# Kernel tuning notes

Measured on AMD Instinct MI355X. Metric: run time of the kernel, lower is better.

The kernel has to match this reference:

```python
import jax, jax.numpy as jnp
import numpy as np

PS = 8          # patch size
D_STATE = 16
D_CONV = 4
DT_RANK = 6     # ceil(96/16)
N_HEADS = 2
NEG = jnp.float32(-1e30)
_DIRS = np.array([[-1, 0], [1, 0], [0, -1], [0, 1]], np.int32)


def _ln(x, w, b, eps=1e-5):
    mu = x.mean(-1, keepdims=True)
    var = ((x - mu) ** 2).mean(-1, keepdims=True)
    return (x - mu) * jax.lax.rsqrt(var + eps) * w + b


def _vit_score_map(x, pos_embed, proj_w, proj_b, in_w, in_b, out_w, out_b,
                   ln1_w, ln1_b, ff1_w, ff1_b, ff2_w, ff2_b, ln2_w, ln2_b,
                   score_w, score_b):
    B, C, H, W = x.shape
    Hp, Wp = H // PS, W // PS
    N = Hp * Wp
    E = proj_w.shape[0]
    # F.unfold ordering: per patch the vector is (C, kr, kc) flattened
    patches = x.reshape(B, C, Hp, PS, Wp, PS).transpose(0, 2, 4, 1, 3, 5).reshape(B, N, C * PS * PS)
    patches = patches @ proj_w.T + proj_b
    if pos_embed.shape[1] != N:
        o = int(pos_embed.shape[1] ** 0.5)
        pe = jax.image.resize(pos_embed.reshape(1, o, o, E), (1, Hp, Wp, E), 'bilinear').reshape(1, N, E)
    else:
        pe = pos_embed
    patches = patches + 0.1 * pe
    # nn.TransformerEncoderLayer defaults: post-norm, ReLU, eval (no dropout)
    qkv = patches @ in_w.T + in_b
    q, k, v = jnp.split(qkv, 3, axis=-1)
    dh = E // N_HEADS
    def heads(t):
        return t.reshape(B, N, N_HEADS, dh).transpose(0, 2, 1, 3)
    q, k, v = heads(q), heads(k), heads(v)
    attn = jax.nn.softmax(jnp.einsum('bhqd,bhkd->bhqk', q, k) / np.float32(np.sqrt(dh)), axis=-1)
    ctx = jnp.einsum('bhqk,bhkd->bhqd', attn, v).transpose(0, 2, 1, 3).reshape(B, N, E)
    src = _ln(patches + (ctx @ out_w.T + out_b), ln1_w, ln1_b)
    ff = jax.nn.relu(src @ ff1_w.T + ff1_b) @ ff2_w.T + ff2_b
    src = _ln(src + ff, ln2_w, ln2_b)
    scores = jax.nn.sigmoid((src @ score_w.T + score_b)[..., 0])
    pvar = patches.var(axis=-1, ddof=1)          # torch.var is unbiased
    final = 0.7 * scores + 0.3 * jax.nn.sigmoid(pvar * 10.0)
    return final.reshape(B, Hp, Wp)


def _traversal(score):
    """Greedy adaptive patch traversal: start at global argmax, walk to the best
    unvisited 4-neighbor; on dead-end jump to the global argmax over unvisited."""
    Hp, Wp = score.shape
    n = Hp * Wp
    s = score.reshape(-1)
    dirs = jnp.asarray(_DIRS)
    start = jnp.argmax(s).astype(jnp.int32)
    visited0 = jnp.zeros((n,), bool).at[start].set(True)

    def step(carry, _):
        visited, cur = carry
        ci, cj = cur // Wp, cur % Wp
        ni, nj = ci + dirs[:, 0], cj + dirs[:, 1]
        valid = (ni >= 0) & (ni < Hp) & (nj >= 0) & (nj < Wp)
        nidx = (jnp.clip(ni, 0, Hp - 1) * Wp + jnp.clip(nj, 0, Wp - 1)).astype(jnp.int32)
        nsc = jnp.where(valid & ~visited[nidx], s[nidx], NEG)
        b = jnp.argmax(nsc)                       # first-max tie-break == '>' loop order
        jump = jnp.argmax(jnp.where(visited, NEG, s)).astype(jnp.int32)
        nxt = jnp.where(nsc[b] > NEG * 0.5, nidx[b], jump).astype(jnp.int32)
        return (visited.at[nxt].set(True), nxt), nxt

    _, rest = jax.lax.scan(step, (visited0, start), None, length=n - 1)
    return jnp.concatenate([start[None], rest])


def _mamba(u, in_w, conv_w, conv_b, xproj_w, dt_w, dt_b, A_log, D_skip, out_w):
    B, L, _ = u.shape
    d_in = conv_w.shape[0]
    xz = u @ in_w.T                               # (B,L,2*d_in)
    xx, z = jnp.split(xz, 2, axis=-1)
    # causal depthwise conv over sequence
    xc = jnp.pad(xx.transpose(0, 2, 1), ((0, 0), (0, 0), (D_CONV - 1, 0)))
    xc = jax.lax.conv_general_dilated(xc, conv_w, (1,), 'VALID',
                                      feature_group_count=d_in,
                                      dimension_numbers=('NCH', 'OIH', 'NCH'))
    xx = jax.nn.silu((xc + conv_b[None, :, None]).transpose(0, 2, 1))   # (B,L,d_in)
    dbl = xx @ xproj_w.T
    dt, Bm, Cm = jnp.split(dbl, [DT_RANK, DT_RANK + D_STATE], axis=-1)
    dt = jax.nn.softplus(dt @ dt_w.T + dt_b)      # (B,L,d_in)
    A = -jnp.exp(A_log)                           # (d_in, d_state)

    def step(h, inp):
        dt_t, B_t, C_t, x_t = inp                 # (B,d_in),(B,ds),(B,ds),(B,d_in)
        h = jnp.exp(dt_t[..., None] * A) * h + (dt_t * x_t)[..., None] * B_t[:, None, :]
        return h, jnp.einsum('bds,bs->bd', h, C_t)

    h0 = jnp.zeros((B, d_in, D_STATE), u.dtype)
    xs = (dt.transpose(1, 0, 2), Bm.transpose(1, 0, 2), Cm.transpose(1, 0, 2), xx.transpose(1, 0, 2))
    _, ys = jax.lax.scan(step, h0, xs)
    y = ys.transpose(1, 0, 2) + xx * D_skip
    return (y * jax.nn.silu(z)) @ out_w.T


def setup_inputs() -> dict:
    key = jax.random.key(0)
    ks = jax.random.split(key, 20)
    B, C, H, W = 2, 96, 128, 128
    E, FF = 96, 2048
    d_in, dr, ds, dc = 192, 6, 16, 4
    f32 = jnp.float32
    def w(k, shape, s=0.02):
        return jax.random.normal(k, shape, f32) * s
    return dict(
        x=jax.random.normal(ks[0], (B, C, H, W), f32),
        pe=w(ks[1], (B, H * W, C), 0.02),
        pos_embed=w(ks[2], (1, 784, E)),
        vit_proj_w=w(ks[3], (E, C * PS * PS)),
        vit_proj_b=jnp.zeros((E,), f32),
        attn_in_w=w(ks[4], (3 * E, E)),
        attn_in_b=jnp.zeros((3 * E,), f32),
        attn_out_w=w(ks[5], (E, E)),
        attn_out_b=jnp.zeros((E,), f32),
        ln1_w=jnp.ones((E,), f32), ln1_b=jnp.zeros((E,), f32),
        ff1_w=w(ks[6], (FF, E)), ff1_b=jnp.zeros((FF,), f32),
        ff2_w=w(ks[7], (E, FF)), ff2_b=jnp.zeros((E,), f32),
        ln2_w=jnp.ones((E,), f32), ln2_b=jnp.zeros((E,), f32),
        score_w=w(ks[8], (1, E)), score_b=jnp.zeros((1,), f32),
        norm_w=jnp.ones((C,), f32), norm_b=jnp.zeros((C,), f32),
        in_proj_w=w(ks[9], (2 * d_in, C)),
        conv_w=w(ks[10], (d_in, 1, dc), 0.1),
        conv_b=jnp.zeros((d_in,), f32),
        x_proj_w=w(ks[11], (dr + 2 * ds, d_in)),
        dt_w=w(ks[12], (d_in, dr)),
        dt_b=jnp.full((d_in,), -4.6, f32),        # softplus(dt_b) ~ 0.01 (mamba dt init)
        A_log=jnp.log(jnp.tile(jnp.arange(1, ds + 1, dtype=f32), (d_in, 1))),
        D_skip=jnp.ones((d_in,), f32),
        out_proj_w=w(ks[13], (C, d_in)),
    )


def reference(x, pe, pos_embed, vit_proj_w, vit_proj_b, attn_in_w, attn_in_b,
              attn_out_w, attn_out_b, ln1_w, ln1_b, ff1_w, ff1_b, ff2_w, ff2_b,
              ln2_w, ln2_b, score_w, score_b, norm_w, norm_b, in_proj_w,
              conv_w, conv_b, x_proj_w, dt_w, dt_b, A_log, D_skip, out_proj_w):
    B, C, H, W = x.shape
    n = H * W
    # Dynamic_Adaptive_Scan with the code's DCNv3Function-is-None fallback:
    # x = input_last, permuted back to channels-first => identity on x.
    x_adapted = x
    score_map = _vit_score_map(x_adapted, pos_embed, vit_proj_w, vit_proj_b,
                               attn_in_w, attn_in_b, attn_out_w, attn_out_b,
                               ln1_w, ln1_b, ff1_w, ff1_b, ff2_w, ff2_b,
                               ln2_w, ln2_b, score_w, score_b)
    order = jax.vmap(_traversal)(jax.lax.stop_gradient(score_map))    # (B, Hp*Wp)
    Hp, Wp = score_map.shape[1], score_map.shape[2]
    pi, pj = order // Wp, order % Wp
    # expand each patch into its PSxPS pixels in raster order
    offs = (jnp.arange(PS, dtype=jnp.int32)[:, None] * W + jnp.arange(PS, dtype=jnp.int32)[None, :]).reshape(-1)
    idx = ((pi * PS * W + pj * PS)[..., None] + offs).reshape(B, n)    # (B, n)
    x_tok = jnp.take_along_axis(x_adapted.reshape(B, C, n), idx[:, None, :], axis=2).transpose(0, 2, 1)
    pe_r = jnp.take_along_axis(pe, idx[..., None], axis=1)
    tokens = _ln(x_tok + pe_r, norm_w, norm_b)
    y = _mamba(tokens, in_proj_w, conv_w, conv_b, x_proj_w, dt_w, dt_b, A_log, D_skip, out_proj_w)
    # scatter back to spatial raster order
    out = jax.vmap(lambda yb, ib: jnp.zeros_like(yb).at[ib].set(yb))(y, idx)
    return out.transpose(0, 2, 1).reshape(B, C, H, W)
```

## Files before the change

### kernel.cpp

```cpp
#include <hip/hip_runtime.h>
#include <math.h>

#define BB 2
#define CC 96
#define HH 128
#define WW 128
#define PS 8
#define HP 16
#define WP 16
#define NPATCH 256
#define EE 96
#define FF 2048
#define DH 48
#define DIN 192
#define DR 6
#define DS 16
#define LL 16384
#define NCHUNK 512
#define CLEN 32
#define NSEG 16
#define SEGC 32
#define KTOT 6144
#define KSPLIT 32
#define KSL 192

__device__ __forceinline__ float sigmoid_acc(float x){ return 1.f/(1.f+expf(-x)); }
__device__ __forceinline__ float sigmoid_fast(float x){ return 1.f/(1.f+__expf(-x)); }

__global__ void k_resize_pe(const float* __restrict__ pos, float* __restrict__ pe16){
  int n = blockIdx.x;
  int oi = n / WP, oj = n % WP;
  int e = threadIdx.x;
  const float inv = 1.75f;
  float sfi = (oi + 0.5f)*inv - 0.5f;
  float sfj = (oj + 0.5f)*inv - 0.5f;
  int i0 = max(0, (int)ceilf(sfi - inv)), i1 = min(27, (int)floorf(sfi + inv));
  int j0 = max(0, (int)ceilf(sfj - inv)), j1 = min(27, (int)floorf(sfj + inv));
  float si = 0.f, sj = 0.f;
  for(int j=i0;j<=i1;j++) si += fmaxf(0.f, 1.f - fabsf(sfi - (float)j)/inv);
  for(int j=j0;j<=j1;j++) sj += fmaxf(0.f, 1.f - fabsf(sfj - (float)j)/inv);
  float acc = 0.f;
  for(int ji=i0;ji<=i1;ji++){
    float wv = fmaxf(0.f, 1.f - fabsf(sfi - (float)ji)/inv) / si;
    for(int jj=j0;jj<=j1;jj++){
      float wu = fmaxf(0.f, 1.f - fabsf(sfj - (float)jj)/inv);
      acc += wv * (wu/sj) * pos[(ji*28+jj)*EE + e];
    }
  }
  pe16[n*EE + e] = acc;
}

__global__ void k_wtr(const float* __restrict__ vw, float* __restrict__ Wt){
  __shared__ float t[64*97];
  int k0 = blockIdx.x*64;
  int tid = threadIdx.x;
  for(int i=tid;i<64*EE;i+=256){
    int e = i>>6, kk = i&63;
    t[kk*97 + e] = vw[(size_t)e*KTOT + k0 + kk];
  }
  __syncthreads();
  for(int i=tid;i<64*EE;i+=256){
    int kk = i/EE, e = i%EE;
    Wt[(size_t)(k0+kk)*EE + e] = t[kk*97 + e];
  }
}

__global__ __launch_bounds__(384) void k_pproj(const float* __restrict__ x,
    const float* __restrict__ Wt, float* __restrict__ part){
  __shared__ float As[16*196];
  int bidx = blockIdx.x;
  int ks = bidx & (KSPLIT-1);
  int pb = bidx >> 5;
  int b = pb >> 4, pi = pb & 15;
  int c0 = ks*3;
  int tid = threadIdx.x;
  for(int i=tid;i<24*128;i+=384){
    int row = i>>7;
    int col = i&127;
    int cl = row>>3, dr = row&7;
    float v = x[(((size_t)(b*CC + c0+cl))<<14) + (size_t)((pi*PS+dr)<<7) + col];
    As[(col>>3)*196 + cl*64 + dr*8 + (col&7)] = v;
  }
  __syncthreads();
  int e = tid % EE;
  int pq = tid / EE;
  const float* wp = Wt + (size_t)(ks*KSL)*EE + e;
  float acc0=0.f, acc1=0.f, acc2=0.f, acc3=0.f;
  const float4* A0 = (const float4*)(As + (pq*4+0)*196);
  const float4* A1 = (const float4*)(As + (pq*4+1)*196);
  const float4* A2 = (const float4*)(As + (pq*4+2)*196);
  const float4* A3 = (const float4*)(As + (pq*4+3)*196);
  #pragma unroll 4
  for(int k4=0;k4<48;k4++){
    float w0 = wp[(k4*4+0)*EE];
    float w1 = wp[(k4*4+1)*EE];
    float w2 = wp[(k4*4+2)*EE];
    float w3 = wp[(k4*4+3)*EE];
    float4 a;
    a = A0[k4]; acc0 += a.x*w0 + a.y*w1 + a.z*w2 + a.w*w3;
    a = A1[k4]; acc1 += a.x*w0 + a.y*w1 + a.z*w2 + a.w*w3;
    a = A2[k4]; acc2 += a.x*w0 + a.y*w1 + a.z*w2 + a.w*w3;
    a = A3[k4]; acc3 += a.x*w0 + a.y*w1 + a.z*w2 + a.w*w3;
  }
  size_t gp0 = (size_t)b*NPATCH + pi*WP + pq*4;
  part[((size_t)ks*512 + gp0+0)*EE + e] = acc0;
  part[((size_t)ks*512 + gp0+1)*EE + e] = acc1;
  part[((size_t)ks*512 + gp0+2)*EE + e] = acc2;
  part[((size_t)ks*512 + gp0+3)*EE + e] = acc3;
}

__global__ __launch_bounds__(320) void k_preduce_qkv(const float* __restrict__ part,
    const float* __restrict__ pb, const float* __restrict__ pe16,
    const float* __restrict__ inw, const float* __restrict__ inb,
    float* __restrict__ patches, float* __restrict__ pvar, float* __restrict__ qkv){
  int gp = blockIdx.x;
  int n = gp % NPATCH;
  int tid = threadIdx.x;
  __shared__ float a[EE];
  __shared__ float ps[2], pq2[2];
  float v = 0.f;
  if(tid < EE){
    float s = 0.f;
    #pragma unroll 8
    for(int ks=0;ks<KSPLIT;ks++) s += part[((size_t)ks*512 + gp)*EE + tid];
    v = s + pb[tid] + 0.1f*pe16[n*EE + tid];
    a[tid] = v;
    patches[(size_t)gp*EE + tid] = v;
  }
  if(tid < 128){
    float sv = v, sq = v*v;
    for(int off=32; off>0; off>>=1){ sv += __shfl_xor(sv, off); sq += __shfl_xor(sq, off); }
    if((tid&63)==0){ ps[tid>>6]=sv; pq2[tid>>6]=sq; }
  }
  __syncthreads();
  if(tid==0){
    float s = ps[0]+ps[1], qq = pq2[0]+pq2[1];
    float mu = s/EE;
    pvar[gp] = (qq - EE*mu*mu)/(EE-1);
  }
  if(tid < 288){
    const float4* ar = (const float4*)a;
    const float4* wr = (const float4*)(inw + (size_t)tid*EE);
    float4 s4 = {0.f,0.f,0.f,0.f};
    #pragma unroll
    for(int k=0;k<24;k++){
      float4 av=ar[k], wv=wr[k];
      s4.x += av.x*wv.x; s4.y += av.y*wv.y; s4.z += av.z*wv.z; s4.w += av.w*wv.w;
    }
    qkv[(size_t)gp*288 + tid] = inb[tid] + (s4.x+s4.y)+(s4.z+s4.w);
  }
}

__global__ __launch_bounds__(256) void k_attn_ln1(const float* __restrict__ qkv,
    const float* __restrict__ ow, const float* __restrict__ ob,
    const float* __restrict__ patches, const float* __restrict__ lw,
    const float* __restrict__ lb, float* __restrict__ src1){
  int gb = blockIdx.x;
  int i = gb & 255, b = gb >> 8;
  int tid = threadIdx.x;
  __shared__ float q[EE];
  __shared__ float2 red[NPATCH];
  __shared__ float p0[NPATCH], p1[NPATCH];
  __shared__ float part[2][EE];
  __shared__ float ctxs[EE];
  __shared__ float ps[2], pq2[2], st[2];
  const float* base = qkv + (size_t)b*NPATCH*288;
  if(tid < EE) q[tid] = base[(size_t)i*288 + tid];
  __syncthreads();
  float sc0, sc1;
  {
    const float4* krow = (const float4*)(base + (size_t)tid*288 + 96);
    const float4* q4 = (const float4*)q;
    float4 a0 = {0.f,0.f,0.f,0.f}, a1 = {0.f,0.f,0.f,0.f};
    #pragma unroll
    for(int k=0;k<12;k++){
      float4 kv=krow[k], qv=q4[k];
      a0.x += qv.x*kv.x; a0.y += qv.y*kv.y; a0.z += qv.z*kv.z; a0.w += qv.w*kv.w;
    }
    #pragma unroll
    for(int k=12;k<24;k++){
      float4 kv=krow[k], qv=q4[k];
      a1.x += qv.x*kv.x; a1.y += qv.y*kv.y; a1.z += qv.z*kv.z; a1.w += qv.w*kv.w;
    }
    sc0 = ((a0.x+a0.y)+(a0.z+a0.w)) * 0.14433756729740643f;
    sc1 = ((a1.x+a1.y)+(a1.z+a1.w)) * 0.14433756729740643f;
  }
  red[tid] = make_float2(sc0, sc1); __syncthreads();
  for(int stp=128; stp>0; stp>>=1){
    if(tid<stp){ float2 o=red[tid+stp]; red[tid].x=fmaxf(red[tid].x,o.x); red[tid].y=fmaxf(red[tid].y,o.y); }
    __syncthreads();
  }
  float2 mx = red[0]; __syncthreads();
  float ev0 = expf(sc0 - mx.x), ev1 = expf(sc1 - mx.y);
  red[tid] = make_float2(ev0, ev1); __syncthreads();
  for(int stp=128; stp>0; stp>>=1){
    if(tid<stp){ float2 o=red[tid+stp]; red[tid].x+=o.x; red[tid].y+=o.y; }
    __syncthreads();
  }
  float2 dn = red[0]; __syncthreads();
  p0[tid] = ev0/dn.x; p1[tid] = ev1/dn.y;
  __syncthreads();
  if(tid < 192){
    int dd = tid % EE, jh = tid / EE;
    const float* vb = base + 192 + dd;
    const float* pp = (dd < DH) ? p0 : p1;
    float acc0 = 0.f, acc1 = 0.f;
    #pragma unroll 4
    for(int j=jh*128; j<jh*128+128; j+=2){
      acc0 += pp[j]*vb[(size_t)j*288];
      acc1 += pp[j+1]*vb[(size_t)(j+1)*288];
    }
    part[jh][dd] = acc0+acc1;
  }
  __syncthreads();
  if(tid < EE) ctxs[tid] = part[0][tid] + part[1][tid];
  __syncthreads();
  float o = 0.f;
  if(tid < EE){
    const float4* ar = (const float4*)ctxs;
    const float4* wr = (const float4*)(ow + (size_t)tid*EE);
    float4 s4 = {0.f,0.f,0.f,0.f};
    #pragma unroll
    for(int k=0;k<24;k++){
      float4 av=ar[k], wv=wr[k];
      s4.x += av.x*wv.x; s4.y += av.y*wv.y; s4.z += av.z*wv.z; s4.w += av.w*wv.w;
    }
    o = ob[tid] + (s4.x+s4.y)+(s4.z+s4.w) + patches[(size_t)gb*EE + tid];
  }
  if(tid < 128){
    float sv = o, sq = o*o;
    for(int off=32; off>0; off>>=1){ sv += __shfl_xor(sv, off); sq += __shfl_xor(sq, off); }
    if((tid&63)==0){ ps[tid>>6]=sv; pq2[tid>>6]=sq; }
  }
  __syncthreads();
  if(tid==0){
    float s = ps[0]+ps[1], qq = pq2[0]+pq2[1];
    float mu = s/EE;
    st[0]=mu; st[1]=rsqrtf(qq/EE - mu*mu + 1e-5f);
  }
  __syncthreads();
  if(tid < EE) src1[(size_t)gb*EE + tid] = (o-st[0])*st[1]*lw[tid] + lb[tid];
}

__global__ __launch_bounds__(512) void k_ff1(const float* __restrict__ src1,
    const float* __restrict__ w1, const float* __restrict__ b1, float* __restrict__ ffh){
  int row0 = blockIdx.x*2; int tid = threadIdx.x;
  const float4* a0 = (const float4*)(src1 + (size_t)row0*EE);
  const float4* a1 = (const float4*)(src1 + (size_t)(row0+1)*EE);
  for(int fo=0;fo<4;fo++){
    int f = fo*512 + tid;
    const float4* wr = (const float4*)(w1 + (size_t)f*EE);
    float bc = b1[f];
    float acc0=bc, acc1=bc;
    #pragma unroll
    for(int k=0;k<24;k++){
      float4 wv = wr[k];
      float4 av;
      av = a0[k]; acc0 += av.x*wv.x+av.y*wv.y+av.z*wv.z+av.w*wv.w;
      av = a1[k]; acc1 += av.x*wv.x+av.y*wv.y+av.z*wv.z+av.w*wv.w;
    }
    ffh[(size_t)(row0+0)*FF + f] = fmaxf(acc0, 0.f);
    ffh[(size_t)(row0+1)*FF + f] = fmaxf(acc1, 0.f);
  }
}

__global__ __launch_bounds__(384) void k_ff2_score(const float* __restrict__ ffh,
    const float* __restrict__ w2, const float* __restrict__ b2,
    const float* __restrict__ src1, const float* __restrict__ lw,
    const float* __restrict__ lb, const float* __restrict__ sw,
    const float* __restrict__ sb, const float* __restrict__ pvar,
    float* __restrict__ fscore){
  __shared__ float partl[8][EE];
  __shared__ float s2[2][EE];
  __shared__ float psr[2][2], pqr[2][2], str[2][2];
  int row0 = blockIdx.x*2; int tid = threadIdx.x;
  int e = tid % EE, fg = tid / EE;
  const float4* wr = (const float4*)(w2 + (size_t)e*FF + fg*512);
  const float4* h0 = (const float4*)(ffh + (size_t)row0*FF + fg*512);
  const float4* h1 = (const float4*)(ffh + (size_t)(row0+1)*FF + fg*512);
  float acc0=0.f, acc1=0.f;
  #pragma unroll 4
  for(int k=0;k<128;k++){
    float4 wv = wr[k];
    float4 hv;
    hv = h0[k]; acc0 += hv.x*wv.x+hv.y*wv.y+hv.z*wv.z+hv.w*wv.w;
    hv = h1[k]; acc1 += hv.x*wv.x+hv.y*wv.y+hv.z*wv.z+hv.w*wv.w;
  }
  partl[0*4+fg][e] = acc0;
  partl[1*4+fg][e] = acc1;
  __syncthreads();
  if(tid < 192){
    int r = tid / EE, e2 = tid % EE;
    float s = partl[r*4+0][e2] + partl[r*4+1][e2] + partl[r*4+2][e2] + partl[r*4+3][e2];
    s2[r][e2] = s + b2[e2] + src1[(size_t)(row0+r)*EE + e2];
  }
  __syncthreads();
  int g = tid >> 7, t = tid & 127;
  float v = 0.f;
  if(g < 2){
    v = (t < EE) ? s2[g][t] : 0.f;
    float sv = v, sq = v*v;
    for(int off=32; off>0; off>>=1){ sv += __shfl_xor(sv, off); sq += __shfl_xor(sq, off); }
    if((t&63)==0){ psr[g][t>>6]=sv; pqr[g][t>>6]=sq; }
  }
  __syncthreads();
  if(g < 2 && t == 0){
    float s = psr[g][0]+psr[g][1], qq = pqr[g][0]+pqr[g][1];
    float mu = s/EE;
    str[g][0]=mu; str[g][1]=rsqrtf(qq/EE - mu*mu + 1e-5f);
  }
  __syncthreads();
  if(g < 2){
    float o = (t < EE) ? ((v-str[g][0])*str[g][1]*lw[t] + lb[t]) * sw[t] : 0.f;
    for(int off=32; off>0; off>>=1) o += __shfl_xor(o, off);
    if((t&63)==0) psr[g][t>>6] = o;
  }
  __syncthreads();
  if(g < 2 && t == 0){
    float acc = psr[g][0]+psr[g][1] + sb[0];
    fscore[row0+g] = 0.7f*sigmoid_acc(acc) + 0.3f*sigmoid_acc(pvar[row0+g]*10.f);
  }
}

__global__ void k_traversal(const float* __restrict__ fscore, int* __restrict__ order){
  int b = blockIdx.x; int lane = threadIdx.x;
  __shared__ float fsl[NPATCH];
  __shared__ int   sidxl[NPATCH];
  __shared__ int   ordl[NPATCH];
  for(int k=lane;k<NPATCH;k+=64) fsl[k] = fscore[b*NPATCH+k];
  __syncthreads();
  {
    float s0=fsl[lane], s1=fsl[64+lane], s2=fsl[128+lane], s3=fsl[192+lane];
    int i0=lane, i1=64+lane, i2=128+lane, i3=192+lane;
    int c0=0,c1=0,c2=0,c3=0;
    for(int j=0;j<NPATCH;j++){
      float sj=fsl[j];
      c0 += (sj>s0 || (sj==s0 && j<i0)) ? 1:0;
      c1 += (sj>s1 || (sj==s1 && j<i1)) ? 1:0;
      c2 += (sj>s2 || (sj==s2 && j<i2)) ? 1:0;
      c3 += (sj>s3 || (sj==s3 && j<i3)) ? 1:0;
    }
    sidxl[c0]=i0; sidxl[c1]=i1; sidxl[c2]=i2; sidxl[c3]=i3;
  }
  __syncthreads();
  if(lane==0){
    int cur = sidxl[0];
    ordl[0] = cur;
    fsl[cur] = -1e30f;
    int ptr = 1;
    int jcand = sidxl[1];
    for(int step=1; step<NPATCH; step++){
      int ci = cur>>4, cj = cur&15;
      int a0 = (ci>0)  ? cur-16 : cur;
      int a1 = (ci<15) ? cur+16 : cur;
      int a2 = (cj>0)  ? cur-1  : cur;
      int a3 = (cj<15) ? cur+1  : cur;
      float n0 = fsl[a0];
      float n1 = fsl[a1];
      float n2 = fsl[a2];
      float n3 = fsl[a3];
      float bv = n0; int bi = a0;
      if(n1 > bv){ bv=n1; bi=a1; }
      if(n2 > bv){ bv=n2; bi=a2; }
      if(n3 > bv){ bv=n3; bi=a3; }
      int nxt = (bv > -1e29f) ? bi : jcand;
      fsl[nxt] = -1e30f;
      ordl[step] = nxt;
      cur = nxt;
      if(nxt == jcand && step < NPATCH-1){
        float jv;
        do { ptr++; jcand = sidxl[ptr]; jv = fsl[jcand]; } while(jv <= -1e29f);
      }
    }
  }
  __syncthreads();
  for(int k=lane;k<NPATCH;k+=64) order[b*NPATCH+k] = ordl[k];
}

__global__ __launch_bounds__(256) void k_gather_ln(const float* __restrict__ x,
    const float* __restrict__ pe, const int* __restrict__ order,
    const float* __restrict__ nw, const float* __restrict__ nb,
    float* __restrict__ tokens){
  __shared__ float val[64*97];
  int gb = blockIdx.x; int b = gb >> 8; int r = gb & 255;
  int tid = threadIdx.x;
  int p = order[b*NPATCH + r]; int pi = p>>4, pj = p&15;
  for(int i=tid;i<96*64;i+=256){
    int c = i>>6, q = i&63;
    int dr = q>>3, dc = q&7;
    val[q*97 + c] = x[(((size_t)(b*CC + c))<<14) + (size_t)((pi*PS+dr)<<7) + pj*PS + dc];
  }
  __syncthreads();
  for(int i=tid;i<64*EE;i+=256){
    int q = i/EE, c = i%EE;
    int pix = ((pi*PS + (q>>3))<<7) + pj*PS + (q&7);
    val[q*97 + c] += pe[((size_t)b*(HH*WW) + pix)*CC + c];
  }
  __syncthreads();
  int wid = tid>>6, lane = tid&63;
  for(int t=wid; t<64; t+=4){
    float v1 = val[t*97 + lane];
    float v2 = (lane<32) ? val[t*97 + 64 + lane] : 0.f;
    float sv = v1+v2, sq = v1*v1 + v2*v2;
    for(int off=32; off>0; off>>=1){ sv += __shfl_xor(sv, off); sq += __shfl_xor(sq, off); }
    float mu = sv/EE;
    float rs = rsqrtf(sq/EE - mu*mu + 1e-5f);
    size_t tb = ((size_t)b*LL + r*64 + t)*EE;
    tokens[tb + lane] = (v1-mu)*rs*nw[lane] + nb[lane];
    if(lane < 32) tokens[tb + 64 + lane] = (v2-mu)*rs*nw[64+lane] + nb[64+lane];
  }
}

__global__ __launch_bounds__(768, 5) void k_inproj_conv(const float* __restrict__ tokens,
    const float* __restrict__ w, const float* __restrict__ cw, const float* __restrict__ cb,
    float* __restrict__ z, float* __restrict__ xc){
  __shared__ float a[35*EE];
  __shared__ float ps[12*384];
  __shared__ float xxl[35*DIN];
  int rb = blockIdx.x; size_t row0 = (size_t)rb*32;
  int l0 = (int)(row0 % LL);
  int tid = threadIdx.x;
  int kh = tid / 384;
  int col = tid - kh*384;
  {
    const float4* src = (const float4*)(tokens + (row0-3)*EE);
    float4* adst = (float4*)a;
    for(int idx=tid; idx<840; idx+=768){
      float4 v;
      if(l0==0 && idx<72){ v.x=0.f; v.y=0.f; v.z=0.f; v.w=0.f; }
      else v = src[idx];
      adst[idx] = v;
    }
  }
  float4 wv[12];
  const float4* wr4 = (const float4*)(w + (size_t)col*EE + kh*48);
  #pragma unroll
  for(int i=0;i<12;i++) wv[i] = wr4[i];
  __syncthreads();
  #pragma unroll
  for(int g=0; g<3; g++){
    float acc[12];
    #pragma unroll
    for(int r=0;r<12;r++){
      int gi = g*12 + r;
      if(gi < 35){
        const float4* ar = (const float4*)(a + gi*EE + kh*48);
        float4 s4 = {0.f,0.f,0.f,0.f};
        #pragma unroll
        for(int i=0;i<12;i++){
          float4 av = ar[i];
          s4.x += av.x*wv[i].x; s4.y += av.y*wv[i].y; s4.z += av.z*wv[i].z; s4.w += av.w*wv[i].w;
        }
        acc[r] = (s4.x+s4.y)+(s4.z+s4.w);
      } else acc[r] = 0.f;
    }
    if(kh==1){
      #pragma unroll
      for(int r=0;r<12;r++) if(g*12+r < 35) ps[r*384 + col] = acc[r];
    }
    __syncthreads();
    if(kh==0){
      #pragma unroll
      for(int r=0;r<12;r++){
        int gi = g*12 + r;
        if(gi < 35){
          float tot = acc[r] + ps[r*384 + col];
          if(col < DIN) xxl[gi*DIN + col] = tot;
          else if(gi >= 3) z[(row0 + gi - 3)*DIN + (col - DIN)] = tot;
        }
      }
    }
    __syncthreads();
  }
  #pragma unroll
  for(int it=0; it<8; it++){
    int idx = tid + it*768;
    int rr = idx / DIN, d = idx - rr*DIN;
    float v = cb[d]
      + cw[d*4+0]*xxl[(rr+0)*DIN + d]
      + cw[d*4+1]*xxl[(rr+1)*DIN + d]
      + cw[d*4+2]*xxl[(rr+2)*DIN + d]
      + cw[d*4+3]*xxl[(rr+3)*DIN + d];
    xc[(row0 + rr)*DIN + d] = v * sigmoid_fast(v);
  }
}

__global__ __launch_bounds__(320) void k_xproj(const float* __restrict__ xc, const float* __restrict__ xpw,
    const float* __restrict__ dtw, const float* __restrict__ dtb,
    float* __restrict__ dt, float* __restrict__ Bm, float* __restrict__ Cm){
  __shared__ float a[8][196];
  __shared__ float dbl[8][40];
  int rb = blockIdx.x; size_t row0 = (size_t)rb*8;
  int tid = threadIdx.x;
  for(int i=tid;i<8*DIN;i+=320){ int r=i/DIN, k=i%DIN; a[r][k] = xc[(row0+r)*DIN + k]; }
  __syncthreads();
  {
    int r = tid & 7, o = tid >> 3;
    if(o < 38){
      const float4* wr = (const float4*)(xpw + (size_t)o*DIN);
      const float4* ar = (const float4*)(a[r]);
      float4 s4 = {0.f,0.f,0.f,0.f};
      #pragma unroll
      for(int k=0;k<48;k++){
        float4 av=ar[k], wv=wr[k];
        s4.x += av.x*wv.x; s4.y += av.y*wv.y; s4.z += av.z*wv.z; s4.w += av.w*wv.w;
      }
      dbl[r][o] = (s4.x+s4.y)+(s4.z+s4.w);
    }
  }
  __syncthreads();
  for(int t=tid;t<8*DIN;t+=320){
    int r = t/DIN, d = t%DIN;
    float acc = dtb[d];
    #pragma unroll
    for(int j=0;j<DR;j++) acc += dbl[r][j]*dtw[d*DR+j];
    dt[(row0+r)*DIN + d] = fmaxf(acc, 0.f) + log1pf(__expf(-fabsf(acc)));
  }
  if(tid < 8*DS){
    int r = tid/DS, s = tid%DS;
    Bm[(row0+r)*DS + s] = dbl[r][6+s];
    Cm[(row0+r)*DS + s] = dbl[r][22+s];
  }
}

__global__ __launch_bounds__(192) void k_scan1(const float* __restrict__ dt,
    const float* __restrict__ xc, const float* __restrict__ Bm,
    const float* __restrict__ Alog, float* __restrict__ hend, float* __restrict__ sumdt){
  int blk = blockIdx.x;
  int b = blk >> 9, c = blk & (NCHUNK-1);
  int d = threadIdx.x;
  float A[16];
  {
    const float4* a4 = (const float4*)(Alog + d*DS);
    #pragma unroll
    for(int i=0;i<4;i++){
      float4 v = a4[i];
      A[i*4+0]=-expf(v.x); A[i*4+1]=-expf(v.y); A[i*4+2]=-expf(v.z); A[i*4+3]=-expf(v.w);
    }
  }
  float h[16];
  #pragma unroll
  for(int s=0;s<16;s++) h[s]=0.f;
  float sd = 0.f;
  size_t base = (size_t)b*LL + (size_t)c*CLEN;
  const float* dp = dt + base*DIN + d;
  const float* xp = xc + base*DIN + d;
  const float4* bp = (const float4*)(Bm + base*DS);
  for(int t=0;t<CLEN;t++){
    float dtv = dp[(size_t)t*DIN];
    float xv  = xp[(size_t)t*DIN];
    float4 b0=bp[t*4+0], b1=bp[t*4+1], b2=bp[t*4+2], b3=bp[t*4+3];
    float e[16];
    #pragma unroll
    for(int s=0;s<16;s++) e[s] = __expf(dtv*A[s]);
    float Bv[16] = {b0.x,b0.y,b0.z,b0.w,b1.x,b1.y,b1.z,b1.w,b2.x,b2.y,b2.z,b2.w,b3.x,b3.y,b3.z,b3.w};
    float dx = dtv*xv; sd += dtv;
    #pragma unroll
    for(int s=0;s<16;s++) h[s] = e[s]*h[s] + dx*Bv[s];
  }
  size_t o = ((size_t)c*BB + b)*DIN + d;
  float4* hp = (float4*)(hend + o*DS);
  hp[0] = make_float4(h[0],h[1],h[2],h[3]);
  hp[1] = make_float4(h[4],h[5],h[6],h[7]);
  hp[2] = make_float4(h[8],h[9],h[10],h[11]);
  hp[3] = make_float4(h[12],h[13],h[14],h[15]);
  sumdt[o] = sd;
}

__global__ __launch_bounds__(256) void k_scan2a(const float* __restrict__ hend,
    const float* __restrict__ sumdt, const float* __restrict__ Alog,
    float* __restrict__ segP, float* __restrict__ segH){
  int g = blockIdx.x*256 + threadIdx.x;
  int seg = g / 6144; int r = g % 6144;
  int b = r / 3072; int d = (r % 3072) >> 4; int s = r & 15;
  float A = -expf(Alog[d*DS + s]);
  float P = 1.f, H = 0.f;
  int c0 = seg*SEGC;
  for(int cc=0; cc<SEGC; cc+=4){
    float sd[4], he[4];
    #pragma unroll
    for(int j=0;j<4;j++){
      size_t o = ((size_t)(c0+cc+j)*BB + b)*DIN + d;
      sd[j] = sumdt[o]; he[j] = hend[o*DS + s];
    }
    #pragma unroll
    for(int j=0;j<4;j++){
      float aa = __expf(A*sd[j]);
      H = aa*H + he[j]; P *= aa;
    }
  }
  segP[seg*6144 + r] = P; segH[seg*6144 + r] = H;
}

__global__ void k_scan2b(const float* __restrict__ segP, const float* __restrict__ segH,
                         float* __restrict__ segHin){
  int r = blockIdx.x*256 + threadIdx.x;
  float P[NSEG], H[NSEG];
  #pragma unroll
  for(int sg=0; sg<NSEG; sg++){ P[sg]=segP[sg*6144+r]; H[sg]=segH[sg*6144+r]; }
  float h = 0.f;
  #pragma unroll
  for(int sg=0; sg<NSEG; sg++){
    segHin[sg*6144 + r] = h;
    h = P[sg]*h + H[sg];
  }
}

__global__ __launch_bounds__(256) void k_scan2c(float* __restrict__ hend,
    const float* __restrict__ sumdt, const float* __restrict__ Alog,
    const float* __restrict__ segHin){
  int g = blockIdx.x*256 + threadIdx.x;
  int seg = g / 6144; int r = g % 6144;
  int b = r / 3072; int d = (r % 3072) >> 4; int s = r & 15;
  float A = -expf(Alog[d*DS + s]);
  float h = segHin[seg*6144 + r];
  int c0 = seg*SEGC;
  for(int cc=0; cc<SEGC; cc+=4){
    float sd[4], he[4]; size_t oo[4];
    #pragma unroll
    for(int j=0;j<4;j++){
      oo[j] = ((size_t)(c0+cc+j)*BB + b)*DIN + d;
      sd[j] = sumdt[oo[j]]; he[j] = hend[oo[j]*DS + s];
    }
    #pragma unroll
    for(int j=0;j<4;j++){
      hend[oo[j]*DS + s] = h;
      float aa = __expf(A*sd[j]);
      h = aa*h + he[j];
    }
  }
}

__global__ __launch_bounds__(192) void k_scan3(const float* __restrict__ dt,
    const float* __restrict__ xc, const float* __restrict__ Bm, const float* __restrict__ Cm,
    const float* __restrict__ Alog, const float* __restrict__ hin,
    const float* __restrict__ Dskip, float* __restrict__ zg){
  int blk = blockIdx.x;
  int b = blk >> 9, c = blk & (NCHUNK-1);
  int d = threadIdx.x;
  float A[16];
  {
    const float4* a4 = (const float4*)(Alog + d*DS);
    #pragma unroll
    for(int i=0;i<4;i++){
      float4 v = a4[i];
      A[i*4+0]=-expf(v.x); A[i*4+1]=-expf(v.y); A[i*4+2]=-expf(v.z); A[i*4+3]=-expf(v.w);
    }
  }
  size_t o = ((size_t)c*BB + b)*DIN + d;
  float h[16];
  {
    const float4* hi = (const float4*)(hin + o*DS);
    #pragma unroll
    for(int i=0;i<4;i++){
      float4 v = hi[i];
      h[i*4+0]=v.x; h[i*4+1]=v.y; h[i*4+2]=v.z; h[i*4+3]=v.w;
    }
  }
  float Dv = Dskip[d];
  size_t base = (size_t)b*LL + (size_t)c*CLEN;
  const float* dp = dt + base*DIN + d;
  const float* xp = xc + base*DIN + d;
  float* zp = zg + base*DIN + d;
  const float4* bp = (const float4*)(Bm + base*DS);
  const float4* cp = (const float4*)(Cm + base*DS);
  for(int t=0;t<CLEN;t++){
    float dtv = dp[(size_t)t*DIN];
    float xv  = xp[(size_t)t*DIN];
    float zv  = zp[(size_t)t*DIN];
    float4 b0=bp[t*4+0], b1=bp[t*4+1], b2=bp[t*4+2], b3=bp[t*4+3];
    float4 c0=cp[t*4+0], c1=cp[t*4+1], c2=cp[t*4+2], c3=cp[t*4+3];
    float e[16];
    #pragma unroll
    for(int s=0;s<16;s++) e[s] = __expf(dtv*A[s]);
    float Bv[16] = {b0.x,b0.y,b0.z,b0.w,b1.x,b1.y,b1.z,b1.w,b2.x,b2.y,b2.z,b2.w,b3.x,b3.y,b3.z,b3.w};
    float Cv[16] = {c0.x,c0.y,c0.z,c0.w,c1.x,c1.y,c1.z,c1.w,c2.x,c2.y,c2.z,c2.w,c3.x,c3.y,c3.z,c3.w};
    float dx = dtv*xv;
    float y = 0.f;
    #pragma unroll
    for(int s=0;s<16;s++){ h[s] = e[s]*h[s] + dx*Bv[s]; y += h[s]*Cv[s]; }
    float yy = y + xv*Dv;
    zp[(size_t)t*DIN] = yy * (zv * sigmoid_fast(zv));
  }
}

__global__ __launch_bounds__(384) void k_outproj(const float* __restrict__ g,
    const float* __restrict__ w, float* __restrict__ ytok){
  __shared__ float a[16*DIN];
  __shared__ float psA[16*EE];
  __shared__ float psB[16*EE];
  int rb = blockIdx.x; size_t row0 = (size_t)rb*16;
  int tid = threadIdx.x;
  int col = tid % EE, kq = tid / EE;
  {
    const float4* src = (const float4*)(g + row0*DIN);
    float4* ad = (float4*)a;
    ad[tid] = src[tid];
    ad[tid+384] = src[tid+384];
  }
  float4 wv[12];
  const float4* wr4 = (const float4*)(w + (size_t)col*DIN + kq*48);
  #pragma unroll
  for(int i=0;i<12;i++) wv[i] = wr4[i];
  __syncthreads();
  float acc[16];
  for(int r=0;r<16;r++){
    const float4* ar = (const float4*)(a + r*DIN + kq*48);
    float4 s4 = {0.f,0.f,0.f,0.f};
    #pragma unroll
    for(int i=0;i<12;i++){
      float4 av = ar[i];
      s4.x += av.x*wv[i].x; s4.y += av.y*wv[i].y; s4.z += av.z*wv[i].z; s4.w += av.w*wv[i].w;
    }
    acc[r] = (s4.x+s4.y)+(s4.z+s4.w);
  }
  if(kq==1){
    for(int r=0;r<16;r++) psA[r*EE+col] = acc[r];
  }
  if(kq==3){
    for(int r=0;r<16;r++) psB[r*EE+col] = acc[r];
  }
  __syncthreads();
  if(kq==0){
    for(int r=0;r<16;r++) acc[r] += psA[r*EE+col];
  }
  if(kq==2){
    for(int r=0;r<16;r++) acc[r] += psB[r*EE+col];
  }
  __syncthreads();
  if(kq==2){
    for(int r=0;r<16;r++) psA[r*EE+col] = acc[r];
  }
  __syncthreads();
  if(kq==0){
    for(int r=0;r<16;r++) ytok[(row0+r)*EE + col] = acc[r] + psA[r*EE+col];
  }
}

__global__ __launch_bounds__(256) void k_scatter(const float* __restrict__ ytok,
    const int* __restrict__ order, float* __restrict__ out){
  __shared__ float yt[64*100];
  int gb = blockIdx.x; int b = gb>>8, r = gb&255;
  int p = order[b*NPATCH + r]; int pi = p>>4, pj = p&15;
  int tid = threadIdx.x;
  for(int i=tid;i<64*24;i+=256){
    int q = i/24, c4 = i%24;
    float4 v = ((const float4*)(ytok + ((size_t)b*LL + r*64 + q)*EE))[c4];
    ((float4*)(yt + q*100))[c4] = v;
  }
  __syncthreads();
  int q = tid&63; int cg = tid>>6;
  int pix = ((pi*PS + (q>>3))<<7) + pj*PS + (q&7);
  for(int c=cg;c<CC;c+=4){
    out[(((size_t)(b*CC + c))<<14) + pix] = yt[q*100 + c];
  }
}

extern "C" void kernel_launch(void* const* d_in, const int* in_sizes, int n_in,
                              void* d_out, int out_size, void* d_ws, size_t ws_size,
                              hipStream_t stream){
  (void)in_sizes; (void)n_in; (void)out_size; (void)ws_size;
  const float* x    = (const float*)d_in[0];
  const float* pe   = (const float*)d_in[1];
  const float* pos  = (const float*)d_in[2];
  const float* vw   = (const float*)d_in[3];
  const float* vb   = (const float*)d_in[4];
  const float* inw  = (const float*)d_in[5];
  const float* inb  = (const float*)d_in[6];
  const float* ow   = (const float*)d_in[7];
  const float* ob   = (const float*)d_in[8];
  const float* l1w  = (const float*)d_in[9];
  const float* l1b  = (const float*)d_in[10];
  const float* f1w  = (const float*)d_in[11];
  const float* f1b  = (const float*)d_in[12];
  const float* f2w  = (const float*)d_in[13];
  const float* f2b  = (const float*)d_in[14];
  const float* l2w  = (const float*)d_in[15];
  const float* l2b  = (const float*)d_in[16];
  const float* sw   = (const float*)d_in[17];
  const float* sb   = (const float*)d_in[18];
  const float* nw   = (const float*)d_in[19];
  const float* nb   = (const float*)d_in[20];
  const float* ipw  = (const float*)d_in[21];
  const float* cw   = (const float*)d_in[22];
  const float* cb   = (const float*)d_in[23];
  const float* xpw  = (const float*)d_in[24];
  const float* dtw  = (const float*)d_in[25];
  const float* dtbp = (const float*)d_in[26];
  const float* alog = (const float*)d_in[27];
  const float* dsk  = (const float*)d_in[28];
  const float* opw  = (const float*)d_in[29];
  float* out = (float*)d_out;

  char* wsb = (char*)d_ws;
  size_t off = 0;
  auto alloc = [&](size_t nfloats)->void*{
    void* p = (void*)(wsb + off);
    off += ((nfloats*sizeof(float) + 255) & ~(size_t)255);
    return p;
  };
  float* pe16    = (float*)alloc(256*96);
  float* patches = (float*)alloc(512*96);
  float* pvar    = (float*)alloc(512);
  float* qkv     = (float*)alloc((size_t)512*288);
  float* src1    = (float*)alloc(512*96);
  float* ffh     = (float*)alloc((size_t)512*2048);
  float* fscore  = (float*)alloc(512);
  int*   order   = (int*)  alloc(512);
  float* tokens  = (float*)alloc((size_t)2*16384*96);
  float* xxb     = (float*)alloc((size_t)2*16384*192);
  float* zb      = (float*)alloc((size_t)2*16384*192);
  float* xcb     = (float*)alloc((size_t)2*16384*192);
  float* Bmat    = (float*)alloc((size_t)2*16384*16);
  float* Cmat    = (float*)alloc((size_t)2*16384*16);
  float* sumdt   = (float*)alloc((size_t)NCHUNK*2*192);
  float* segP    = (float*)alloc((size_t)NSEG*6144);
  float* segH    = (float*)alloc((size_t)NSEG*6144);
  float* segHin  = (float*)alloc((size_t)NSEG*6144);
  float* dtbuf = xxb;
  float* Wt    = xxb;
  float* part  = tokens;
  float* hend  = tokens;
  float* hin   = hend;
  float* ytok  = tokens;

  k_resize_pe   <<<256,   96, 0, stream>>>(pos, pe16);
  k_wtr         <<<96,   256, 0, stream>>>(vw, Wt);
  k_pproj       <<<1024, 384, 0, stream>>>(x, Wt, part);
  k_preduce_qkv <<<512,  320, 0, stream>>>(part, vb, pe16, inw, inb, patches, pvar, qkv);
  k_attn_ln1    <<<512,  256, 0, stream>>>(qkv, ow, ob, patches, l1w, l1b, src1);
  k_ff1         <<<256,  512, 0, stream>>>(src1, f1w, f1b, ffh);
  k_ff2_score   <<<256,  384, 0, stream>>>(ffh, f2w, f2b, src1, l2w, l2b, sw, sb, pvar, fscore);
  k_traversal   <<<2,     64, 0, stream>>>(fscore, order);
  k_gather_ln   <<<512,  256, 0, stream>>>(x, pe, order, nw, nb, tokens);
  k_inproj_conv <<<1024, 768, 0, stream>>>(tokens, ipw, cw, cb, zb, xcb);
  k_xproj       <<<4096, 320, 0, stream>>>(xcb, xpw, dtw, dtbp, dtbuf, Bmat, Cmat);
  k_scan1       <<<1024, 192, 0, stream>>>(dtbuf, xcb, Bmat, alog, hend, sumdt);
  k_scan2a      <<<384,  256, 0, stream>>>(hend, sumdt, alog, segP, segH);
  k_scan2b      <<<24,   256, 0, stream>>>(segP, segH, segHin);
  k_scan2c      <<<384,  256, 0, stream>>>(hend, sumdt, alog, segHin);
  k_scan3       <<<1024, 192, 0, stream>>>(dtbuf, xcb, Bmat, Cmat, alog, hin, dsk, zb);
  k_outproj     <<<2048, 384, 0, stream>>>(zb, opw, ytok);
  k_scatter     <<<512,  256, 0, stream>>>(ytok, order, out);
}
```

Measured before the change: 504.3 us.

## Run LayerNorm and in-projection in raster order, overlapped with the traversal

LayerNorm and the in-projection act on each token independently, so they now run in spatial raster order in the same launch as the greedy traversal. Two blocks compute the traversal and write a per-token pixel map, while the remaining blocks normalise and project pixels straight from the input. The depthwise conv then gathers projected rows through the pixel map, and scan3 reads and writes the gate buffer at raster positions. This makes the outproj output already raster-ordered, so the final scatter becomes a plain transpose. The aim is to hide the serial single-thread traversal behind useful work and drop the separate gather pass, at the cost of indirect, less coalesced row accesses in the conv and in scan3.

Result: faster. 448.7 us (-11.0%).

```diff
diff --git a/kernel.cpp b/kernel.cpp
--- a/kernel.cpp
+++ b/kernel.cpp
@@ -322,166 +322,172 @@
   }
 }
 
-__global__ void k_traversal(const float* __restrict__ fscore, int* __restrict__ order){
-  int b = blockIdx.x; int lane = threadIdx.x;
+__global__ __launch_bounds__(768) void k_trav_fused(const float* __restrict__ fscore,
+    const float* __restrict__ x, const float* __restrict__ pe,
+    const float* __restrict__ nw, const float* __restrict__ nb,
+    const float* __restrict__ w, int* __restrict__ pixmap,
+    float* __restrict__ xx, float* __restrict__ z){
   __shared__ float fsl[NPATCH];
   __shared__ int   sidxl[NPATCH];
   __shared__ int   ordl[NPATCH];
-  for(int k=lane;k<NPATCH;k+=64) fsl[k] = fscore[b*NPATCH+k];
-  __syncthreads();
-  {
-    float s0=fsl[lane], s1=fsl[64+lane], s2=fsl[128+lane], s3=fsl[192+lane];
-    int i0=lane, i1=64+lane, i2=128+lane, i3=192+lane;
-    int c0=0,c1=0,c2=0,c3=0;
-    for(int j=0;j<NPATCH;j++){
-      float sj=fsl[j];
-      c0 += (sj>s0 || (sj==s0 && j<i0)) ? 1:0;
-      c1 += (sj>s1 || (sj==s1 && j<i1)) ? 1:0;
-      c2 += (sj>s2 || (sj==s2 && j<i2)) ? 1:0;
-      c3 += (sj>s3 || (sj==s3 && j<i3)) ? 1:0;
-    }
-    sidxl[c0]=i0; sidxl[c1]=i1; sidxl[c2]=i2; sidxl[c3]=i3;
-  }
-  __syncthreads();
-  if(lane==0){
-    int cur = sidxl[0];
-    ordl[0] = cur;
-    fsl[cur] = -1e30f;
-    int ptr = 1;
-    int jcand = sidxl[1];
-    for(int step=1; step<NPATCH; step++){
-      int ci = cur>>4, cj = cur&15;
-      int a0 = (ci>0)  ? cur-16 : cur;
-      int a1 = (ci<15) ? cur+16 : cur;
-      int a2 = (cj>0)  ? cur-1  : cur;
-      int a3 = (cj<15) ? cur+1  : cur;
-      float n0 = fsl[a0];
-      float n1 = fsl[a1];
-      float n2 = fsl[a2];
-      float n3 = fsl[a3];
-      float bv = n0; int bi = a0;
-      if(n1 > bv){ bv=n1; bi=a1; }
-      if(n2 > bv){ bv=n2; bi=a2; }
-      if(n3 > bv){ bv=n3; bi=a3; }
-      int nxt = (bv > -1e29f) ? bi : jcand;
-      fsl[nxt] = -1e30f;
-      ordl[step] = nxt;
-      cur = nxt;
-      if(nxt == jcand && step < NPATCH-1){
-        float jv;
-        do { ptr++; jcand = sidxl[ptr]; jv = fsl[jcand]; } while(jv <= -1e29f);
+  __shared__ float a[32*100];
+  __shared__ float ps[12*384];
+  int tid = threadIdx.x;
+  if(blockIdx.x < 2){
+    int b = blockIdx.x;
+    int lane = tid;
+    if(lane < 64){
+      for(int k=lane;k<NPATCH;k+=64) fsl[k] = fscore[b*NPATCH+k];
+    }
+    __syncthreads();
+    if(lane < 64){
+      float s0=fsl[lane], s1=fsl[64+lane], s2=fsl[128+lane], s3=fsl[192+lane];
+      int i0=lane, i1=64+lane, i2=128+lane, i3=192+lane;
+      int c0=0,c1=0,c2=0,c3=0;
+      for(int j=0;j<NPATCH;j++){
+        float sj=fsl[j];
+        c0 += (sj>s0 || (sj==s0 && j<i0)) ? 1:0;
+        c1 += (sj>s1 || (sj==s1 && j<i1)) ? 1:0;
+        c2 += (sj>s2 || (sj==s2 && j<i2)) ? 1:0;
+        c3 += (sj>s3 || (sj==s3 && j<i3)) ? 1:0;
       }
-    }
-  }
-  __syncthreads();
-  for(int k=lane;k<NPATCH;k+=64) order[b*NPATCH+k] = ordl[k];
-}
-
-__global__ __launch_bounds__(256) void k_gather_ln(const float* __restrict__ x,
-    const float* __restrict__ pe, const int* __restrict__ order,
-    const float* __restrict__ nw, const float* __restrict__ nb,
-    float* __restrict__ tokens){
-  __shared__ float val[64*97];
-  int gb = blockIdx.x; int b = gb >> 8; int r = gb & 255;
-  int tid = threadIdx.x;
-  int p = order[b*NPATCH + r]; int pi = p>>4, pj = p&15;
-  for(int i=tid;i<96*64;i+=256){
-    int c = i>>6, q = i&63;
-    int dr = q>>3, dc = q&7;
-    val[q*97 + c] = x[(((size_t)(b*CC + c))<<14) + (size_t)((pi*PS+dr)<<7) + pj*PS + dc];
-  }
-  __syncthreads();
-  for(int i=tid;i<64*EE;i+=256){
-    int q = i/EE, c = i%EE;
-    int pix = ((pi*PS + (q>>3))<<7) + pj*PS + (q&7);
-    val[q*97 + c] += pe[((size_t)b*(HH*WW) + pix)*CC + c];
-  }
-  __syncthreads();
-  int wid = tid>>6, lane = tid&63;
-  for(int t=wid; t<64; t+=4){
-    float v1 = val[t*97 + lane];
-    float v2 = (lane<32) ? val[t*97 + 64 + lane] : 0.f;
-    float sv = v1+v2, sq = v1*v1 + v2*v2;
-    for(int off=32; off>0; off>>=1){ sv += __shfl_xor(sv, off); sq += __shfl_xor(sq, off); }
-    float mu = sv/EE;
-    float rs = rsqrtf(sq/EE - mu*mu + 1e-5f);
-    size_t tb = ((size_t)b*LL + r*64 + t)*EE;
-    tokens[tb + lane] = (v1-mu)*rs*nw[lane] + nb[lane];
-    if(lane < 32) tokens[tb + 64 + lane] = (v2-mu)*rs*nw[64+lane] + nb[64+lane];
-  }
-}
-
-__global__ __launch_bounds__(768, 5) void k_inproj_conv(const float* __restrict__ tokens,
-    const float* __restrict__ w, const float* __restrict__ cw, const float* __restrict__ cb,
-    float* __restrict__ z, float* __restrict__ xc){
-  __shared__ float a[35*EE];
-  __shared__ float ps[12*384];
-  __shared__ float xxl[35*DIN];
-  int rb = blockIdx.x; size_t row0 = (size_t)rb*32;
-  int l0 = (int)(row0 % LL);
-  int tid = threadIdx.x;
-  int kh = tid / 384;
-  int col = tid - kh*384;
-  {
-    const float4* src = (const float4*)(tokens + (row0-3)*EE);
-    float4* adst = (float4*)a;
-    for(int idx=tid; idx<840; idx+=768){
-      float4 v;
-      if(l0==0 && idx<72){ v.x=0.f; v.y=0.f; v.z=0.f; v.w=0.f; }
-      else v = src[idx];
-      adst[idx] = v;
-    }
-  }
-  float4 wv[12];
-  const float4* wr4 = (const float4*)(w + (size_t)col*EE + kh*48);
-  #pragma unroll
-  for(int i=0;i<12;i++) wv[i] = wr4[i];
-  __syncthreads();
-  #pragma unroll
-  for(int g=0; g<3; g++){
-    float acc[12];
-    #pragma unroll
-    for(int r=0;r<12;r++){
-      int gi = g*12 + r;
-      if(gi < 35){
-        const float4* ar = (const float4*)(a + gi*EE + kh*48);
-        float4 s4 = {0.f,0.f,0.f,0.f};
-        #pragma unroll
-        for(int i=0;i<12;i++){
-          float4 av = ar[i];
-          s4.x += av.x*wv[i].x; s4.y += av.y*wv[i].y; s4.z += av.z*wv[i].z; s4.w += av.w*wv[i].w;
+      sidxl[c0]=i0; sidxl[c1]=i1; sidxl[c2]=i2; sidxl[c3]=i3;
+    }
+    __syncthreads();
+    if(lane==0){
+      int cur = sidxl[0];
+      ordl[0] = cur;
+      fsl[cur] = -1e30f;
+      int ptr = 1;
+      int jcand = sidxl[1];
+      for(int step=1; step<NPATCH; step++){
+        int ci = cur>>4, cj = cur&15;
+        int a0 = (ci>0)  ? cur-16 : cur;
+        int a1 = (ci<15) ? cur+16 : cur;
+        int a2 = (cj>0)  ? cur-1  : cur;
+        int a3 = (cj<15) ? cur+1  : cur;
+        float n0 = fsl[a0];
+        float n1 = fsl[a1];
+        float n2 = fsl[a2];
+        float n3 = fsl[a3];
+        float bv = n0; int bi = a0;
+        if(n1 > bv){ bv=n1; bi=a1; }
+        if(n2 > bv){ bv=n2; bi=a2; }
+        if(n3 > bv){ bv=n3; bi=a3; }
+        int nxt = (bv > -1e29f) ? bi : jcand;
+        fsl[nxt] = -1e30f;
+        ordl[step] = nxt;
+        cur = nxt;
+        if(nxt == jcand && step < NPATCH-1){
+          float jv;
+          do { ptr++; jcand = sidxl[ptr]; jv = fsl[jcand]; } while(jv <= -1e29f);
         }
-        acc[r] = (s4.x+s4.y)+(s4.z+s4.w);
-      } else acc[r] = 0.f;
-    }
-    if(kh==1){
-      #pragma unroll
-      for(int r=0;r<12;r++) if(g*12+r < 35) ps[r*384 + col] = acc[r];
+      }
     }
     __syncthreads();
-    if(kh==0){
+    for(int l=tid; l<LL; l+=768){
+      int r = l>>6, q = l&63;
+      int p = ordl[r];
+      pixmap[b*LL + l] = (((p>>4)*PS + (q>>3))<<7) + (p&15)*PS + (q&7);
+    }
+  } else {
+    int rb = blockIdx.x - 2;
+    int R0 = rb*32;
+    int b = R0 >> 14;
+    int p0 = R0 & 16383;
+    for(int i=tid;i<3072;i+=768){
+      int c = i>>5, pl = i&31;
+      a[pl*100 + c] = x[(((size_t)(b*CC + c))<<14) + p0 + pl];
+    }
+    __syncthreads();
+    for(int i=tid;i<3072;i+=768){
+      int pl = i/96, c = i - pl*96;
+      a[pl*100 + c] += pe[((size_t)b*(HH*WW) + p0 + pl)*CC + c];
+    }
+    __syncthreads();
+    {
+      int wid = tid>>6, lane = tid&63;
+      for(int t=wid; t<32; t+=12){
+        float v1 = a[t*100 + lane];
+        float v2 = (lane<32) ? a[t*100 + 64 + lane] : 0.f;
+        float sv = v1+v2, sq = v1*v1 + v2*v2;
+        for(int off=32; off>0; off>>=1){ sv += __shfl_xor(sv, off); sq += __shfl_xor(sq, off); }
+        float mu = sv/EE;
+        float rs = rsqrtf(sq/EE - mu*mu + 1e-5f);
+        a[t*100 + lane] = (v1-mu)*rs*nw[lane] + nb[lane];
+        if(lane < 32) a[t*100 + 64 + lane] = (v2-mu)*rs*nw[64+lane] + nb[64+lane];
+      }
+    }
+    __syncthreads();
+    int kh = tid/384, col = tid - kh*384;
+    float4 wv[12];
+    const float4* wr4 = (const float4*)(w + (size_t)col*EE + kh*48);
+    #pragma unroll
+    for(int i=0;i<12;i++) wv[i] = wr4[i];
+    #pragma unroll
+    for(int g=0; g<3; g++){
+      float acc[12];
       #pragma unroll
       for(int r=0;r<12;r++){
         int gi = g*12 + r;
-        if(gi < 35){
-          float tot = acc[r] + ps[r*384 + col];
-          if(col < DIN) xxl[gi*DIN + col] = tot;
-          else if(gi >= 3) z[(row0 + gi - 3)*DIN + (col - DIN)] = tot;
+        if(gi < 32){
+          const float4* ar = (const float4*)(a + gi*100 + kh*48);
+          float4 s4 = {0.f,0.f,0.f,0.f};
+          #pragma unroll
+          for(int i=0;i<12;i++){
+            float4 av = ar[i];
+            s4.x += av.x*wv[i].x; s4.y += av.y*wv[i].y; s4.z += av.z*wv[i].z; s4.w += av.w*wv[i].w;
+          }
+          acc[r] = (s4.x+s4.y)+(s4.z+s4.w);
+        } else acc[r] = 0.f;
+      }
+      if(kh==1){
+        #pragma unroll
+        for(int r=0;r<12;r++) if(g*12+r < 32) ps[r*384 + col] = acc[r];
+      }
+      __syncthreads();
+      if(kh==0){
+        #pragma unroll
+        for(int r=0;r<12;r++){
+          int gi = g*12 + r;
+          if(gi < 32){
+            float tot = acc[r] + ps[r*384 + col];
+            if(col < DIN) xx[(size_t)(R0 + gi)*DIN + col] = tot;
+            else          z [(size_t)(R0 + gi)*DIN + (col - DIN)] = tot;
+          }
         }
       }
-    }
-    __syncthreads();
-  }
-  #pragma unroll
-  for(int it=0; it<8; it++){
-    int idx = tid + it*768;
-    int rr = idx / DIN, d = idx - rr*DIN;
+      __syncthreads();
+    }
+  }
+}
+
+__global__ __launch_bounds__(256) void k_convgather(const float* __restrict__ xx,
+    const int* __restrict__ pixmap, const float* __restrict__ cw,
+    const float* __restrict__ cb, float* __restrict__ xc){
+  __shared__ int pixl[35];
+  __shared__ float xxl[35*DIN];
+  int blk = blockIdx.x; int b = blk>>9; int l0 = (blk&511)*32;
+  int tid = threadIdx.x;
+  if(tid < 35){
+    int l = l0 - 3 + tid;
+    pixl[tid] = (l >= 0) ? pixmap[b*LL + l] : 0;
+  }
+  __syncthreads();
+  for(int i=tid; i<35*DIN; i+=256){
+    int rr = i/DIN, d = i - rr*DIN;
+    int l = l0 - 3 + rr;
+    xxl[i] = (l >= 0) ? xx[((size_t)b*LL + pixl[rr])*DIN + d] : 0.f;
+  }
+  __syncthreads();
+  for(int i=tid; i<32*DIN; i+=256){
+    int rr = i/DIN, d = i - rr*DIN;
     float v = cb[d]
       + cw[d*4+0]*xxl[(rr+0)*DIN + d]
       + cw[d*4+1]*xxl[(rr+1)*DIN + d]
       + cw[d*4+2]*xxl[(rr+2)*DIN + d]
       + cw[d*4+3]*xxl[(rr+3)*DIN + d];
-    xc[(row0 + rr)*DIN + d] = v * sigmoid_fast(v);
+    xc[((size_t)b*LL + l0 + rr)*DIN + d] = v * sigmoid_fast(v);
   }
 }
 
@@ -634,10 +640,13 @@
 __global__ __launch_bounds__(192) void k_scan3(const float* __restrict__ dt,
     const float* __restrict__ xc, const float* __restrict__ Bm, const float* __restrict__ Cm,
     const float* __restrict__ Alog, const float* __restrict__ hin,
-    const float* __restrict__ Dskip, float* __restrict__ zg){
+    const float* __restrict__ Dskip, const int* __restrict__ pixmap,
+    float* __restrict__ z){
+  __shared__ int pixs[CLEN];
   int blk = blockIdx.x;
   int b = blk >> 9, c = blk & (NCHUNK-1);
   int d = threadIdx.x;
+  if(d < CLEN) pixs[d] = pixmap[b*LL + c*CLEN + d];
   float A[16];
   {
     const float4* a4 = (const float4*)(Alog + d*DS);
@@ -661,13 +670,14 @@
   size_t base = (size_t)b*LL + (size_t)c*CLEN;
   const float* dp = dt + base*DIN + d;
   const float* xp = xc + base*DIN + d;
-  float* zp = zg + base*DIN + d;
   const float4* bp = (const float4*)(Bm + base*DS);
   const float4* cp = (const float4*)(Cm + base*DS);
+  __syncthreads();
   for(int t=0;t<CLEN;t++){
     float dtv = dp[(size_t)t*DIN];
     float xv  = xp[(size_t)t*DIN];
-    float zv  = zp[(size_t)t*DIN];
+    size_t zrow = ((size_t)b*LL + pixs[t])*DIN + d;
+    float zv  = z[zrow];
     float4 b0=bp[t*4+0], b1=bp[t*4+1], b2=bp[t*4+2], b3=bp[t*4+3];
     float4 c0=cp[t*4+0], c1=cp[t*4+1], c2=cp[t*4+2], c3=cp[t*4+3];
     float e[16];
@@ -680,7 +690,7 @@
     #pragma unroll
     for(int s=0;s<16;s++){ h[s] = e[s]*h[s] + dx*Bv[s]; y += h[s]*Cv[s]; }
     float yy = y + xv*Dv;
-    zp[(size_t)t*DIN] = yy * (zv * sigmoid_fast(zv));
+    z[zrow] = yy * (zv * sigmoid_fast(zv));
   }
 }
 
@@ -738,19 +748,18 @@
 }
 
 __global__ __launch_bounds__(256) void k_scatter(const float* __restrict__ ytok,
-    const int* __restrict__ order, float* __restrict__ out){
+    float* __restrict__ out){
   __shared__ float yt[64*100];
-  int gb = blockIdx.x; int b = gb>>8, r = gb&255;
-  int p = order[b*NPATCH + r]; int pi = p>>4, pj = p&15;
+  int gb = blockIdx.x; int b = gb>>8, ch = gb&255;
   int tid = threadIdx.x;
   for(int i=tid;i<64*24;i+=256){
     int q = i/24, c4 = i%24;
-    float4 v = ((const float4*)(ytok + ((size_t)b*LL + r*64 + q)*EE))[c4];
+    float4 v = ((const float4*)(ytok + ((size_t)b*LL + ch*64 + q)*EE))[c4];
     ((float4*)(yt + q*100))[c4] = v;
   }
   __syncthreads();
   int q = tid&63; int cg = tid>>6;
-  int pix = ((pi*PS + (q>>3))<<7) + pj*PS + (q&7);
+  int pix = ch*64 + q;
   for(int c=cg;c<CC;c+=4){
     out[(((size_t)(b*CC + c))<<14) + pix] = yt[q*100 + c];
   }
@@ -806,7 +815,7 @@
   float* src1    = (float*)alloc(512*96);
   float* ffh     = (float*)alloc((size_t)512*2048);
   float* fscore  = (float*)alloc(512);
-  int*   order   = (int*)  alloc(512);
+  int*   pixmap  = (int*)  alloc((size_t)2*16384);
   float* tokens  = (float*)alloc((size_t)2*16384*96);
   float* xxb     = (float*)alloc((size_t)2*16384*192);
   float* zb      = (float*)alloc((size_t)2*16384*192);
@@ -831,15 +840,14 @@
   k_attn_ln1    <<<512,  256, 0, stream>>>(qkv, ow, ob, patches, l1w, l1b, src1);
   k_ff1         <<<256,  512, 0, stream>>>(src1, f1w, f1b, ffh);
   k_ff2_score   <<<256,  384, 0, stream>>>(ffh, f2w, f2b, src1, l2w, l2b, sw, sb, pvar, fscore);
-  k_traversal   <<<2,     64, 0, stream>>>(fscore, order);
-  k_gather_ln   <<<512,  256, 0, stream>>>(x, pe, order, nw, nb, tokens);
-  k_inproj_conv <<<1024, 768, 0, stream>>>(tokens, ipw, cw, cb, zb, xcb);
+  k_trav_fused  <<<1026, 768, 0, stream>>>(fscore, x, pe, nw, nb, ipw, pixmap, xxb, zb);
+  k_convgather  <<<1024, 256, 0, stream>>>(xxb, pixmap, cw, cb, xcb);
   k_xproj       <<<4096, 320, 0, stream>>>(xcb, xpw, dtw, dtbp, dtbuf, Bmat, Cmat);
   k_scan1       <<<1024, 192, 0, stream>>>(dtbuf, xcb, Bmat, alog, hend, sumdt);
   k_scan2a      <<<384,  256, 0, stream>>>(hend, sumdt, alog, segP, segH);
   k_scan2b      <<<24,   256, 0, stream>>>(segP, segH, segHin);
   k_scan2c      <<<384,  256, 0, stream>>>(hend, sumdt, alog, segHin);
-  k_scan3       <<<1024, 192, 0, stream>>>(dtbuf, xcb, Bmat, Cmat, alog, hin, dsk, zb);
+  k_scan3       <<<1024, 192, 0, stream>>>(dtbuf, xcb, Bmat, Cmat, alog, hin, dsk, pixmap, zb);
   k_outproj     <<<2048, 384, 0, stream>>>(zb, opw, ytok);
-  k_scatter     <<<512,  256, 0, stream>>>(ytok, order, out);
-}
+  k_scatter     <<<512,  256, 0, stream>>>(ytok, out);
+}
```
